# Performance work log

Hardware: AMD Instinct MI355X
Metric: run time of the kernel (lower is better)

## Reference

```python
import jax, jax.numpy as jnp
import numpy as np

B, S, D, GH = 8, 1024, 768, 32
THETA = 0.01


def _mlp(params, h):
    # DeepMemoryMLP (2 layers): Linear -> SiLU -> Linear
    W1, b1, W2, b2 = params
    h1 = jax.nn.silu(h @ W1.T + b1)
    return h1 @ W2.T + b2


def setup_inputs() -> dict:
    key = jax.random.key(0)
    ks = jax.random.split(key, 12)
    n = lambda k, sh, std=0.02: std * jax.random.normal(k, sh, dtype=jnp.float32)
    return {
        "x": jax.random.normal(ks[0], (B, S, D), dtype=jnp.float32),
        "WK_w": n(ks[1], (D, D)), "WK_b": jnp.zeros((D,), jnp.float32),
        "WV_w": n(ks[2], (D, D)), "WV_b": jnp.zeros((D,), jnp.float32),
        "WQ_w": n(ks[3], (D, D)), "WQ_b": jnp.zeros((D,), jnp.float32),
        "M_W1": n(ks[4], (D, D)), "M_b1": jnp.zeros((D,), jnp.float32),
        "M_W2": n(ks[5], (D, D)), "M_b2": jnp.zeros((D,), jnp.float32),
        "FG_W1": n(ks[6], (GH, D), std=float(1.0 / np.sqrt(D))), "FG_b1": jnp.zeros((GH,), jnp.float32),
        "FG_w2": n(ks[7], (1, GH), std=float(1.0 / np.sqrt(GH))), "FG_b2": jnp.zeros((1,), jnp.float32),
        "DG_W1": n(ks[8], (GH, D), std=float(1.0 / np.sqrt(D))), "DG_b1": jnp.zeros((GH,), jnp.float32),
        "DG_w2": n(ks[9], (1, GH), std=float(1.0 / np.sqrt(GH))), "DG_b2": jnp.zeros((1,), jnp.float32),
    }


def reference(x, WK_w, WK_b, WV_w, WV_b, WQ_w, WQ_b,
              M_W1, M_b1, M_W2, M_b2,
              FG_W1, FG_b1, FG_w2, FG_b2,
              DG_W1, DG_b1, DG_w2, DG_b2):
    # Projections (Eq. 12 inputs): k_t, v_t per token; q for retrieval
    k = jnp.einsum('bsd,ed->bse', x, WK_w) + WK_b   # [B,S,D]
    v = jnp.einsum('bsd,ed->bse', x, WV_w) + WV_b
    q = jnp.einsum('bsd,ed->bse', x, WQ_w) + WQ_b

    def gate(W1, b1, w2, b2):
        h = jax.nn.silu(jnp.einsum('bsd,hd->bsh', x, W1) + b1)
        return jax.nn.sigmoid(jnp.einsum('bsh,oh->bso', h, w2) + b2)[..., 0]  # [B,S]

    alpha = gate(FG_W1, FG_b1, FG_w2, FG_b2).mean(axis=0)  # [S] forget gate per step
    eta = gate(DG_W1, DG_b1, DG_w2, DG_b2).mean(axis=0)    # [S] momentum decay per step

    params0 = (M_W1, M_b1, M_W2, M_b2)
    S0 = jax.tree_util.tree_map(jnp.zeros_like, params0)   # momentum buffer

    def loss_fn(p, kt, vt):
        # l(M; x) = ||M(k_t) - v_t||^2 (MSE over the batch of tokens at step t)
        return jnp.mean((_mlp(p, kt) - vt) ** 2)

    def step(carry, inputs):
        p, s = carry
        kt, vt, a_t, e_t = inputs  # kt, vt: [B,D]
        g = jax.grad(loss_fn)(p, kt, vt)
        # Eq. 13: S_t = eta_t * S_{t-1} - theta * grad
        s = jax.tree_util.tree_map(lambda si, gi: e_t * si - THETA * gi, s, g)
        # Eq. 14: M_t = (1 - alpha_t) * M_{t-1} + S_t
        p = jax.tree_util.tree_map(lambda pi, si: (1.0 - a_t) * pi + si, p, s)
        return (p, s), None

    kt = jnp.swapaxes(k, 0, 1)  # [S,B,D]
    vt = jnp.swapaxes(v, 0, 1)
    (p_final, _), _ = jax.lax.scan(step, (params0, S0), (kt, vt, alpha, eta))

    # Retrieval with updated memory: out = M_T(q)
    return _mlp(p_final, q)
```

## Files before the change

kernel.cpp:

```cpp
#include <hip/hip_runtime.h>
#include <math.h>


#define S_LEN 1024
#define D_DIM 768
#define B_SZ 8
#define NWG 256
#define NTHR 192
#define THETA_F 0.01f
#define FLAG_STRIDE 16

__device__ __forceinline__ void st_agent(float* p, float v) {
  __hip_atomic_store(p, v, __ATOMIC_RELAXED, __HIP_MEMORY_SCOPE_AGENT);
}

template <int ACT, int REMAP>
__global__ __launch_bounds__(256) void gemm_tn(const float* __restrict__ A,
                                               const float* __restrict__ W,
                                               const float* __restrict__ bias,
                                               float* __restrict__ C) {
  __shared__ float As[16][132];
  __shared__ float Ws[16][68];
  const int tid = threadIdx.x;
  const int txx = tid & 15, tyy = tid >> 4;
  const int eb = blockIdx.x * 64;
  const int nb = blockIdx.y * 128;
  float acc[8][4];
#pragma unroll
  for (int i = 0; i < 8; ++i)
#pragma unroll
    for (int j = 0; j < 4; ++j) acc[i][j] = 0.f;

  const int lr = tid >> 2;
  const int lc = (tid & 3) << 2;

  for (int k0 = 0; k0 < 768; k0 += 16) {
    float4 a0 = *(const float4*)(A + (size_t)(nb + lr) * 768 + k0 + lc);
    float4 a1 = *(const float4*)(A + (size_t)(nb + lr + 64) * 768 + k0 + lc);
    float4 wv = *(const float4*)(W + (size_t)(eb + lr) * 768 + k0 + lc);
    __syncthreads();
    As[lc + 0][lr] = a0.x; As[lc + 1][lr] = a0.y; As[lc + 2][lr] = a0.z; As[lc + 3][lr] = a0.w;
    As[lc + 0][lr + 64] = a1.x; As[lc + 1][lr + 64] = a1.y; As[lc + 2][lr + 64] = a1.z; As[lc + 3][lr + 64] = a1.w;
    Ws[lc + 0][lr] = wv.x; Ws[lc + 1][lr] = wv.y; Ws[lc + 2][lr] = wv.z; Ws[lc + 3][lr] = wv.w;
    __syncthreads();
#pragma unroll
    for (int kk = 0; kk < 16; ++kk) {
      float4 x0 = *(const float4*)(&As[kk][tyy * 8]);
      float4 x1 = *(const float4*)(&As[kk][tyy * 8 + 4]);
      float4 y0 = *(const float4*)(&Ws[kk][txx * 4]);
      float a8[8] = {x0.x, x0.y, x0.z, x0.w, x1.x, x1.y, x1.z, x1.w};
      float b4[4] = {y0.x, y0.y, y0.z, y0.w};
#pragma unroll
      for (int i = 0; i < 8; ++i)
#pragma unroll
        for (int j = 0; j < 4; ++j) acc[i][j] = fmaf(a8[i], b4[j], acc[i][j]);
    }
  }
  float4 bv = *(const float4*)(bias + eb + txx * 4);
#pragma unroll
  for (int i = 0; i < 8; ++i) {
    int n = nb + tyy * 8 + i;
    float4 o;
    o.x = acc[i][0] + bv.x; o.y = acc[i][1] + bv.y;
    o.z = acc[i][2] + bv.z; o.w = acc[i][3] + bv.w;
    if (ACT == 1) {
      o.x = o.x / (1.f + expf(-o.x));
      o.y = o.y / (1.f + expf(-o.y));
      o.z = o.z / (1.f + expf(-o.z));
      o.w = o.w / (1.f + expf(-o.w));
    }
    size_t row = REMAP ? (size_t)((n & 1023) * 8 + (n >> 10)) : (size_t)n;
    *(float4*)(C + row * 768 + eb + txx * 4) = o;
  }
}

__global__ __launch_bounds__(512) void gates_kernel(
    const float* __restrict__ x, const float* __restrict__ FGW1,
    const float* __restrict__ FGb1, const float* __restrict__ FGw2,
    const float* __restrict__ FGb2, const float* __restrict__ DGW1,
    const float* __restrict__ DGb1, const float* __restrict__ DGw2,
    const float* __restrict__ DGb2, float* __restrict__ alphaA,
    float* __restrict__ etaA) {
  __shared__ float sA[8], sE[8];
  const int t = blockIdx.x, tid = threadIdx.x;
  const int b = tid >> 6, lane = tid & 63;
  const bool isFG = lane < 32;
  const int h = lane & 31;
  const float* xr = x + ((size_t)b * S_LEN + t) * D_DIM;
  const float* Wr = (isFG ? FGW1 : DGW1) + (size_t)h * D_DIM;
  float acc = 0.f;
  for (int d = 0; d < D_DIM; d += 4) {
    float4 xv = *(const float4*)(xr + d);
    float4 wv = *(const float4*)(Wr + d);
    acc = fmaf(xv.x, wv.x, acc);
    acc = fmaf(xv.y, wv.y, acc);
    acc = fmaf(xv.z, wv.z, acc);
    acc = fmaf(xv.w, wv.w, acc);
  }
  float z = acc + (isFG ? FGb1[h] : DGb1[h]);
  float sg = 1.f / (1.f + expf(-z));
  float p = z * sg * (isFG ? FGw2[h] : DGw2[h]);
#pragma unroll
  for (int off = 16; off > 0; off >>= 1) p += __shfl_xor(p, off, 64);
  if (lane == 0) sA[b] = 1.f / (1.f + expf(-(p + FGb2[0])));
  if (lane == 32) sE[b] = 1.f / (1.f + expf(-(p + DGb2[0])));
  __syncthreads();
  if (tid == 0) {
    float sa = 0.f, se = 0.f;
#pragma unroll
    for (int i = 0; i < 8; ++i) { sa += sA[i]; se += sE[i]; }
    alphaA[t] = sa * 0.125f;
    etaA[t] = se * 0.125f;
  }
}

__device__ __forceinline__ void grid_barrier(int* arrive, int* go, int wg,
                                             int tid, int epoch) {
  __syncthreads();
  if (wg == 0) {
#pragma unroll 1
    for (int s = tid + 1; s < NWG; s += NTHR) {
      while (__hip_atomic_load(arrive + s * FLAG_STRIDE, __ATOMIC_RELAXED,
                               __HIP_MEMORY_SCOPE_AGENT) < epoch) {
        __builtin_amdgcn_s_sleep(1);
      }
    }
    __syncthreads();
    if (tid == 0)
      __hip_atomic_store(go, epoch, __ATOMIC_RELAXED,
                         __HIP_MEMORY_SCOPE_AGENT);
  } else {
    if (tid == 0) {
      __hip_atomic_store(arrive + wg * FLAG_STRIDE, epoch, __ATOMIC_RELAXED,
                         __HIP_MEMORY_SCOPE_AGENT);
      while (__hip_atomic_load(go, __ATOMIC_RELAXED,
                               __HIP_MEMORY_SCOPE_AGENT) < epoch) {
        __builtin_amdgcn_s_sleep(1);
      }
    }
    __syncthreads();
  }
}

__device__ __forceinline__ void stage_tile(const float* gsrc, float* sdst,
                                           int tid) {
  const unsigned long long* src = (const unsigned long long*)gsrc;
  unsigned long long u[16];
#pragma unroll
  for (int j = 0; j < 16; ++j)
    u[j] = __hip_atomic_load(src + tid + j * 192, __ATOMIC_RELAXED,
                             __HIP_MEMORY_SCOPE_AGENT);
  unsigned long long* dst = (unsigned long long*)sdst;
#pragma unroll
  for (int j = 0; j < 16; ++j) dst[tid + j * 192] = u[j];
}

__global__ __launch_bounds__(NTHR, 1) void scan_kernel(
    const float* __restrict__ kbuf, const float* __restrict__ vbuf,
    const float* __restrict__ alphaA, const float* __restrict__ etaA,
    const float* __restrict__ MW1, const float* __restrict__ Mb1,
    const float* __restrict__ MW2, const float* __restrict__ Mb2,
    float* __restrict__ W1f, float* __restrict__ b1f, float* __restrict__ W2f,
    float* __restrict__ b2f, float* h1g, float* dOg,
    int* arrive, int* go) {
  __shared__ float sW1[3][768], sS1[3][768], sW2[3][768], sS2[3][768];
  __shared__ float sW2T[3][768], sS2T[3][768];
  __shared__ float sTile[6144];
  __shared__ float sb1[3], ssb1[3], sb2[3], ssb2[3];

  const int tid = threadIdx.x, wg = blockIdx.x;
  const int r = tid >> 6, lane = tid & 63;
  const int jg = wg * 3 + r;
  const int colb = lane * 12;

  {
    const float4* s1 = (const float4*)(MW1 + (size_t)jg * 768 + colb);
    float4* d1 = (float4*)(&sW1[r][colb]);
    d1[0] = s1[0]; d1[1] = s1[1]; d1[2] = s1[2];
    const float4* s2 = (const float4*)(MW2 + (size_t)jg * 768 + colb);
    float4* d2 = (float4*)(&sW2[r][colb]);
    d2[0] = s2[0]; d2[1] = s2[1]; d2[2] = s2[2];
#pragma unroll
    for (int m = 0; m < 12; ++m)
      sW2T[r][colb + m] = MW2[(size_t)(colb + m) * 768 + jg];
    float4 z4 = {0.f, 0.f, 0.f, 0.f};
    ((float4*)&sS1[r][colb])[0] = z4; ((float4*)&sS1[r][colb])[1] = z4; ((float4*)&sS1[r][colb])[2] = z4;
    ((float4*)&sS2[r][colb])[0] = z4; ((float4*)&sS2[r][colb])[1] = z4; ((float4*)&sS2[r][colb])[2] = z4;
    ((float4*)&sS2T[r][colb])[0] = z4; ((float4*)&sS2T[r][colb])[1] = z4; ((float4*)&sS2T[r][colb])[2] = z4;
    if (lane == 0) {
      sb1[r] = Mb1[jg]; sb2[r] = Mb2[jg];
      ssb1[r] = 0.f; ssb2[r] = 0.f;
    }
  }
  __syncthreads();

  int epoch = 0;
  alignas(16) float ktv[8][12];
  float hprev[8], sgv[8], h1loc[8];
  const float c0 = 2.0f / 6144.0f;

  for (int t = 0; t < S_LEN; ++t) {
    const float a_t = alphaA[t], e_t = etaA[t];
    const float om_a = 1.0f - a_t;

#pragma unroll
    for (int b = 0; b < 8; ++b) {
      const float4* kp =
          (const float4*)(kbuf + ((size_t)t * 8 + b) * 768 + colb);
      float4 k0 = kp[0], k1 = kp[1], k2 = kp[2];
      ktv[b][0] = k0.x; ktv[b][1] = k0.y; ktv[b][2] = k0.z; ktv[b][3] = k0.w;
      ktv[b][4] = k1.x; ktv[b][5] = k1.y; ktv[b][6] = k1.z; ktv[b][7] = k1.w;
      ktv[b][8] = k2.x; ktv[b][9] = k2.y; ktv[b][10] = k2.z; ktv[b][11] = k2.w;
    }

    {
      alignas(16) float w1v[12];
      const float4* wp = (const float4*)(&sW1[r][colb]);
      *(float4*)&w1v[0] = wp[0]; *(float4*)&w1v[4] = wp[1]; *(float4*)&w1v[8] = wp[2];
      float acc[8] = {0, 0, 0, 0, 0, 0, 0, 0};
#pragma unroll
      for (int m = 0; m < 12; ++m)
#pragma unroll
        for (int b = 0; b < 8; ++b) acc[b] = fmaf(ktv[b][m], w1v[m], acc[b]);
#pragma unroll
      for (int off = 32; off > 0; off >>= 1)
#pragma unroll
        for (int b = 0; b < 8; ++b) acc[b] += __shfl_xor(acc[b], off, 64);
      const float b1v = sb1[r];
#pragma unroll
      for (int b = 0; b < 8; ++b) {
        float z = acc[b] + b1v;
        float sg = 1.0f / (1.0f + expf(-z));
        hprev[b] = z; sgv[b] = sg; h1loc[b] = z * sg;
      }
#pragma unroll
      for (int b = 0; b < 8; ++b)
        if (lane == b) st_agent(h1g + b * 768 + jg, h1loc[b]);
    }
    grid_barrier(arrive, go, wg, tid, ++epoch);

    {
      stage_tile(h1g, sTile, tid);
      __syncthreads();
      alignas(16) float w2v[12];
      const float4* wp = (const float4*)(&sW2[r][colb]);
      *(float4*)&w2v[0] = wp[0]; *(float4*)&w2v[4] = wp[1]; *(float4*)&w2v[8] = wp[2];
      alignas(16) float hc[8][12];
#pragma unroll
      for (int b = 0; b < 8; ++b) {
        const float4* hp = (const float4*)(&sTile[b * 768 + colb]);
        float4 h0 = hp[0], h1 = hp[1], h2 = hp[2];
        hc[b][0] = h0.x; hc[b][1] = h0.y; hc[b][2] = h0.z; hc[b][3] = h0.w;
        hc[b][4] = h1.x; hc[b][5] = h1.y; hc[b][6] = h1.z; hc[b][7] = h1.w;
        hc[b][8] = h2.x; hc[b][9] = h2.y; hc[b][10] = h2.z; hc[b][11] = h2.w;
      }
      float acc[8] = {0, 0, 0, 0, 0, 0, 0, 0};
#pragma unroll
      for (int m = 0; m < 12; ++m)
#pragma unroll
        for (int b = 0; b < 8; ++b) acc[b] = fmaf(hc[b][m], w2v[m], acc[b]);
#pragma unroll
      for (int off = 32; off > 0; off >>= 1)
#pragma unroll
        for (int b = 0; b < 8; ++b) acc[b] += __shfl_xor(acc[b], off, 64);
      const float b2v = sb2[r];
      float dOv[8];
#pragma unroll
      for (int b = 0; b < 8; ++b) {
        float outv = acc[b] + b2v;
        dOv[b] = c0 * (outv - vbuf[((size_t)t * 8 + b) * 768 + jg]);
      }
#pragma unroll
      for (int b = 0; b < 8; ++b)
        if (lane == b) st_agent(dOg + b * 768 + jg, dOv[b]);
#pragma unroll
      for (int m = 0; m < 12; ++m) {
        float g = 0.f;
#pragma unroll
        for (int b = 0; b < 8; ++b) g = fmaf(dOv[b], hc[b][m], g);
        float snew = e_t * sS2[r][colb + m] - THETA_F * g;
        sS2[r][colb + m] = snew;
        sW2[r][colb + m] = om_a * w2v[m] + snew;
      }
      if (lane == 0) {
        float gb = dOv[0] + dOv[1] + dOv[2] + dOv[3] + dOv[4] + dOv[5] + dOv[6] + dOv[7];
        float snew = e_t * ssb2[r] - THETA_F * gb;
        ssb2[r] = snew;
        sb2[r] = om_a * sb2[r] + snew;
      }
    }
    grid_barrier(arrive, go, wg, tid, ++epoch);

    {
      stage_tile(dOg, sTile, tid);
      __syncthreads();
      alignas(16) float w2tv[12];
      const float4* wp = (const float4*)(&sW2T[r][colb]);
      *(float4*)&w2tv[0] = wp[0]; *(float4*)&w2tv[4] = wp[1]; *(float4*)&w2tv[8] = wp[2];
      alignas(16) float dc[8][12];
#pragma unroll
      for (int b = 0; b < 8; ++b) {
        const float4* dp = (const float4*)(&sTile[b * 768 + colb]);
        float4 d0 = dp[0], d1 = dp[1], d2 = dp[2];
        dc[b][0] = d0.x; dc[b][1] = d0.y; dc[b][2] = d0.z; dc[b][3] = d0.w;
        dc[b][4] = d1.x; dc[b][5] = d1.y; dc[b][6] = d1.z; dc[b][7] = d1.w;
        dc[b][8] = d2.x; dc[b][9] = d2.y; dc[b][10] = d2.z; dc[b][11] = d2.w;
      }
      float acc[8] = {0, 0, 0, 0, 0, 0, 0, 0};
#pragma unroll
      for (int m = 0; m < 12; ++m)
#pragma unroll
        for (int b = 0; b < 8; ++b) acc[b] = fmaf(dc[b][m], w2tv[m], acc[b]);
#pragma unroll
      for (int off = 32; off > 0; off >>= 1)
#pragma unroll
        for (int b = 0; b < 8; ++b) acc[b] += __shfl_xor(acc[b], off, 64);
      float dpre[8];
#pragma unroll
      for (int b = 0; b < 8; ++b)
        dpre[b] = acc[b] * (sgv[b] * (1.0f + hprev[b] * (1.0f - sgv[b])));
#pragma unroll
      for (int m = 0; m < 12; ++m) {
        float g = 0.f;
#pragma unroll
        for (int b = 0; b < 8; ++b) g = fmaf(dpre[b], ktv[b][m], g);
        float snew = e_t * sS1[r][colb + m] - THETA_F * g;
        sS1[r][colb + m] = snew;
        sW1[r][colb + m] = om_a * sW1[r][colb + m] + snew;
      }
#pragma unroll
      for (int m = 0; m < 12; ++m) {
        float g = 0.f;
#pragma unroll
        for (int b = 0; b < 8; ++b) g = fmaf(h1loc[b], dc[b][m], g);
        float snew = e_t * sS2T[r][colb + m] - THETA_F * g;
        sS2T[r][colb + m] = snew;
        sW2T[r][colb + m] = om_a * sW2T[r][colb + m] + snew;
      }
      if (lane == 0) {
        float gb = dpre[0] + dpre[1] + dpre[2] + dpre[3] + dpre[4] + dpre[5] + dpre[6] + dpre[7];
        float snew = e_t * ssb1[r] - THETA_F * gb;
        ssb1[r] = snew;
        sb1[r] = om_a * sb1[r] + snew;
      }
    }
  }

  {
    float4* d1 = (float4*)(W1f + (size_t)jg * 768 + colb);
    const float4* s1 = (const float4*)(&sW1[r][colb]);
    d1[0] = s1[0]; d1[1] = s1[1]; d1[2] = s1[2];
    float4* d2 = (float4*)(W2f + (size_t)jg * 768 + colb);
    const float4* s2 = (const float4*)(&sW2[r][colb]);
    d2[0] = s2[0]; d2[1] = s2[1]; d2[2] = s2[2];
    if (lane == 0) {
      b1f[jg] = sb1[r];
      b2f[jg] = sb2[r];
    }
  }
}

extern "C" void kernel_launch(void* const* d_in, const int* in_sizes, int n_in,
                              void* d_out, int out_size, void* d_ws,
                              size_t ws_size, hipStream_t stream) {
  (void)in_sizes; (void)n_in; (void)out_size; (void)ws_size;
  const float* x   = (const float*)d_in[0];
  const float* WKw = (const float*)d_in[1];
  const float* WKb = (const float*)d_in[2];
  const float* WVw = (const float*)d_in[3];
  const float* WVb = (const float*)d_in[4];
  const float* WQw = (const float*)d_in[5];
  const float* WQb = (const float*)d_in[6];
  const float* MW1 = (const float*)d_in[7];
  const float* Mb1 = (const float*)d_in[8];
  const float* MW2 = (const float*)d_in[9];
  const float* Mb2 = (const float*)d_in[10];
  const float* FGW1 = (const float*)d_in[11];
  const float* FGb1 = (const float*)d_in[12];
  const float* FGw2 = (const float*)d_in[13];
  const float* FGb2 = (const float*)d_in[14];
  const float* DGW1 = (const float*)d_in[15];
  const float* DGb1 = (const float*)d_in[16];
  const float* DGw2 = (const float*)d_in[17];
  const float* DGb2 = (const float*)d_in[18];
  float* out = (float*)d_out;

  float* ws = (float*)d_ws;
  float* kbuf = ws;
  float* vbuf = ws + 6291456;
  float* W1f  = ws + 12582912;
  float* W2f  = W1f + 589824;
  float* b1f  = W2f + 589824;
  float* b2f  = b1f + 768;
  float* alphaA = b2f + 768;
  float* etaA   = alphaA + 1024;
  float* h1g  = etaA + 1024;
  float* dOg  = h1g + 6144;
  int* arrive = (int*)(dOg + 6144);
  int* go     = arrive + NWG * FLAG_STRIDE;
  float* qbuf = kbuf;
  float* h1q  = vbuf;

  hipMemsetAsync(arrive, 0, (NWG * FLAG_STRIDE + FLAG_STRIDE) * sizeof(int),
                 stream);

  dim3 gg(12, 64), bb(256);
  gemm_tn<0, 1><<<gg, bb, 0, stream>>>(x, WKw, WKb, kbuf);
  gemm_tn<0, 1><<<gg, bb, 0, stream>>>(x, WVw, WVb, vbuf);
  gates_kernel<<<dim3(1024), dim3(512), 0, stream>>>(
      x, FGW1, FGb1, FGw2, FGb2, DGW1, DGb1, DGw2, DGb2, alphaA, etaA);
  scan_kernel<<<dim3(NWG), dim3(NTHR), 0, stream>>>(
      kbuf, vbuf, alphaA, etaA, MW1, Mb1, MW2, Mb2, W1f, b1f, W2f, b2f, h1g,
      dOg, arrive, go);
  gemm_tn<0, 0><<<gg, bb, 0, stream>>>(x, WQw, WQb, qbuf);
  gemm_tn<1, 0><<<gg, bb, 0, stream>>>(qbuf, W1f, b1f, h1q);
  gemm_tn<0, 0><<<gg, bb, 0, stream>>>(h1q, W2f, b2f, out);
}
```

Before: 12.57 ms.

## Keep per-row memory weights and momentum in registers with fewer, larger workgroups

The persistent scan kernel now keeps each wavefront's slice of W1, W2, W2ᵀ and their momentum buffers in registers instead of shared memory. It launches 128 workgroups of 384 threads (6 rows each) instead of 256 of 192, which halves the number of participants in every grid barrier. k_t is re-read from global memory in the backward step rather than held in registers, to limit register pressure. This removes the shared-memory traffic for weight updates and cuts barrier fan-in, at the cost of higher register use per thread and an extra global read of k each step.

```diff
diff --git a/kernel.cpp b/kernel.cpp
--- a/kernel.cpp
+++ b/kernel.cpp
@@ -5,13 +5,26 @@
 #define S_LEN 1024
 #define D_DIM 768
 #define B_SZ 8
-#define NWG 256
-#define NTHR 192
+#define NWG 128
+#define NTHR 384
 #define THETA_F 0.01f
 #define FLAG_STRIDE 16
 
 __device__ __forceinline__ void st_agent(float* p, float v) {
   __hip_atomic_store(p, v, __ATOMIC_RELAXED, __HIP_MEMORY_SCOPE_AGENT);
+}
+
+__device__ __forceinline__ void load12(const float* __restrict__ p, float* d) {
+  float4 a = ((const float4*)p)[0], b = ((const float4*)p)[1],
+         c = ((const float4*)p)[2];
+  d[0]=a.x; d[1]=a.y; d[2]=a.z; d[3]=a.w;
+  d[4]=b.x; d[5]=b.y; d[6]=b.z; d[7]=b.w;
+  d[8]=c.x; d[9]=c.y; d[10]=c.z; d[11]=c.w;
+}
+__device__ __forceinline__ void store12(float* __restrict__ p, const float* s) {
+  ((float4*)p)[0] = make_float4(s[0], s[1], s[2], s[3]);
+  ((float4*)p)[1] = make_float4(s[4], s[5], s[6], s[7]);
+  ((float4*)p)[2] = make_float4(s[8], s[9], s[10], s[11]);
 }
 
 template <int ACT, int REMAP>
@@ -145,14 +158,14 @@
 __device__ __forceinline__ void stage_tile(const float* gsrc, float* sdst,
                                            int tid) {
   const unsigned long long* src = (const unsigned long long*)gsrc;
-  unsigned long long u[16];
-#pragma unroll
-  for (int j = 0; j < 16; ++j)
-    u[j] = __hip_atomic_load(src + tid + j * 192, __ATOMIC_RELAXED,
+  unsigned long long u[8];
+#pragma unroll
+  for (int j = 0; j < 8; ++j)
+    u[j] = __hip_atomic_load(src + tid + j * NTHR, __ATOMIC_RELAXED,
                              __HIP_MEMORY_SCOPE_AGENT);
   unsigned long long* dst = (unsigned long long*)sdst;
 #pragma unroll
-  for (int j = 0; j < 16; ++j) dst[tid + j * 192] = u[j];
+  for (int j = 0; j < 8; ++j) dst[tid + j * NTHR] = u[j];
 }
 
 __global__ __launch_bounds__(NTHR, 1) void scan_kernel(
@@ -163,39 +176,24 @@
     float* __restrict__ W1f, float* __restrict__ b1f, float* __restrict__ W2f,
     float* __restrict__ b2f, float* h1g, float* dOg,
     int* arrive, int* go) {
-  __shared__ float sW1[3][768], sS1[3][768], sW2[3][768], sS2[3][768];
-  __shared__ float sW2T[3][768], sS2T[3][768];
   __shared__ float sTile[6144];
-  __shared__ float sb1[3], ssb1[3], sb2[3], ssb2[3];
 
   const int tid = threadIdx.x, wg = blockIdx.x;
-  const int r = tid >> 6, lane = tid & 63;
-  const int jg = wg * 3 + r;
+  const int w = tid >> 6, lane = tid & 63;
+  const int jg = wg * 6 + w;
   const int colb = lane * 12;
 
-  {
-    const float4* s1 = (const float4*)(MW1 + (size_t)jg * 768 + colb);
-    float4* d1 = (float4*)(&sW1[r][colb]);
-    d1[0] = s1[0]; d1[1] = s1[1]; d1[2] = s1[2];
-    const float4* s2 = (const float4*)(MW2 + (size_t)jg * 768 + colb);
-    float4* d2 = (float4*)(&sW2[r][colb]);
-    d2[0] = s2[0]; d2[1] = s2[1]; d2[2] = s2[2];
-#pragma unroll
-    for (int m = 0; m < 12; ++m)
-      sW2T[r][colb + m] = MW2[(size_t)(colb + m) * 768 + jg];
-    float4 z4 = {0.f, 0.f, 0.f, 0.f};
-    ((float4*)&sS1[r][colb])[0] = z4; ((float4*)&sS1[r][colb])[1] = z4; ((float4*)&sS1[r][colb])[2] = z4;
-    ((float4*)&sS2[r][colb])[0] = z4; ((float4*)&sS2[r][colb])[1] = z4; ((float4*)&sS2[r][colb])[2] = z4;
-    ((float4*)&sS2T[r][colb])[0] = z4; ((float4*)&sS2T[r][colb])[1] = z4; ((float4*)&sS2T[r][colb])[2] = z4;
-    if (lane == 0) {
-      sb1[r] = Mb1[jg]; sb2[r] = Mb2[jg];
-      ssb1[r] = 0.f; ssb2[r] = 0.f;
-    }
-  }
-  __syncthreads();
+  float w1[12], s1[12], w2[12], s2[12], w2t[12], s2t[12];
+  load12(MW1 + (size_t)jg * 768 + colb, w1);
+  load12(MW2 + (size_t)jg * 768 + colb, w2);
+#pragma unroll
+  for (int m = 0; m < 12; ++m) {
+    w2t[m] = MW2[(size_t)(colb + m) * 768 + jg];
+    s1[m] = 0.f; s2[m] = 0.f; s2t[m] = 0.f;
+  }
+  float b1v = Mb1[jg], b2v = Mb2[jg], sb1v = 0.f, sb2v = 0.f;
 
   int epoch = 0;
-  alignas(16) float ktv[8][12];
   float hprev[8], sgv[8], h1loc[8];
   const float c0 = 2.0f / 6144.0f;
 
@@ -203,30 +201,21 @@
     const float a_t = alphaA[t], e_t = etaA[t];
     const float om_a = 1.0f - a_t;
 
-#pragma unroll
-    for (int b = 0; b < 8; ++b) {
-      const float4* kp =
-          (const float4*)(kbuf + ((size_t)t * 8 + b) * 768 + colb);
-      float4 k0 = kp[0], k1 = kp[1], k2 = kp[2];
-      ktv[b][0] = k0.x; ktv[b][1] = k0.y; ktv[b][2] = k0.z; ktv[b][3] = k0.w;
-      ktv[b][4] = k1.x; ktv[b][5] = k1.y; ktv[b][6] = k1.z; ktv[b][7] = k1.w;
-      ktv[b][8] = k2.x; ktv[b][9] = k2.y; ktv[b][10] = k2.z; ktv[b][11] = k2.w;
-    }
-
     {
-      alignas(16) float w1v[12];
-      const float4* wp = (const float4*)(&sW1[r][colb]);
-      *(float4*)&w1v[0] = wp[0]; *(float4*)&w1v[4] = wp[1]; *(float4*)&w1v[8] = wp[2];
-      float acc[8] = {0, 0, 0, 0, 0, 0, 0, 0};
-#pragma unroll
-      for (int m = 0; m < 12; ++m)
-#pragma unroll
-        for (int b = 0; b < 8; ++b) acc[b] = fmaf(ktv[b][m], w1v[m], acc[b]);
+      float acc[8];
+#pragma unroll
+      for (int b = 0; b < 8; ++b) {
+        float kv[12];
+        load12(kbuf + ((size_t)t * 8 + b) * 768 + colb, kv);
+        float a = 0.f;
+#pragma unroll
+        for (int m = 0; m < 12; ++m) a = fmaf(kv[m], w1[m], a);
+        acc[b] = a;
+      }
 #pragma unroll
       for (int off = 32; off > 0; off >>= 1)
 #pragma unroll
         for (int b = 0; b < 8; ++b) acc[b] += __shfl_xor(acc[b], off, 64);
-      const float b1v = sb1[r];
 #pragma unroll
       for (int b = 0; b < 8; ++b) {
         float z = acc[b] + b1v;
@@ -242,75 +231,62 @@
     {
       stage_tile(h1g, sTile, tid);
       __syncthreads();
-      alignas(16) float w2v[12];
-      const float4* wp = (const float4*)(&sW2[r][colb]);
-      *(float4*)&w2v[0] = wp[0]; *(float4*)&w2v[4] = wp[1]; *(float4*)&w2v[8] = wp[2];
-      alignas(16) float hc[8][12];
-#pragma unroll
-      for (int b = 0; b < 8; ++b) {
-        const float4* hp = (const float4*)(&sTile[b * 768 + colb]);
-        float4 h0 = hp[0], h1 = hp[1], h2 = hp[2];
-        hc[b][0] = h0.x; hc[b][1] = h0.y; hc[b][2] = h0.z; hc[b][3] = h0.w;
-        hc[b][4] = h1.x; hc[b][5] = h1.y; hc[b][6] = h1.z; hc[b][7] = h1.w;
-        hc[b][8] = h2.x; hc[b][9] = h2.y; hc[b][10] = h2.z; hc[b][11] = h2.w;
-      }
-      float acc[8] = {0, 0, 0, 0, 0, 0, 0, 0};
-#pragma unroll
-      for (int m = 0; m < 12; ++m)
-#pragma unroll
-        for (int b = 0; b < 8; ++b) acc[b] = fmaf(hc[b][m], w2v[m], acc[b]);
+      float acc[8];
+#pragma unroll
+      for (int b = 0; b < 8; ++b) {
+        float hv[12];
+        load12(&sTile[b * 768 + colb], hv);
+        float a = 0.f;
+#pragma unroll
+        for (int m = 0; m < 12; ++m) a = fmaf(hv[m], w2[m], a);
+        acc[b] = a;
+      }
 #pragma unroll
       for (int off = 32; off > 0; off >>= 1)
 #pragma unroll
         for (int b = 0; b < 8; ++b) acc[b] += __shfl_xor(acc[b], off, 64);
-      const float b2v = sb2[r];
       float dOv[8];
 #pragma unroll
       for (int b = 0; b < 8; ++b) {
         float outv = acc[b] + b2v;
         dOv[b] = c0 * (outv - vbuf[((size_t)t * 8 + b) * 768 + jg]);
-      }
-#pragma unroll
-      for (int b = 0; b < 8; ++b)
         if (lane == b) st_agent(dOg + b * 768 + jg, dOv[b]);
+      }
+      float gm[12];
+#pragma unroll
+      for (int m = 0; m < 12; ++m) gm[m] = 0.f;
+#pragma unroll
+      for (int b = 0; b < 8; ++b) {
+        float hv[12];
+        load12(&sTile[b * 768 + colb], hv);
+#pragma unroll
+        for (int m = 0; m < 12; ++m) gm[m] = fmaf(dOv[b], hv[m], gm[m]);
+      }
 #pragma unroll
       for (int m = 0; m < 12; ++m) {
-        float g = 0.f;
-#pragma unroll
-        for (int b = 0; b < 8; ++b) g = fmaf(dOv[b], hc[b][m], g);
-        float snew = e_t * sS2[r][colb + m] - THETA_F * g;
-        sS2[r][colb + m] = snew;
-        sW2[r][colb + m] = om_a * w2v[m] + snew;
-      }
-      if (lane == 0) {
-        float gb = dOv[0] + dOv[1] + dOv[2] + dOv[3] + dOv[4] + dOv[5] + dOv[6] + dOv[7];
-        float snew = e_t * ssb2[r] - THETA_F * gb;
-        ssb2[r] = snew;
-        sb2[r] = om_a * sb2[r] + snew;
-      }
+        s2[m] = e_t * s2[m] - THETA_F * gm[m];
+        w2[m] = om_a * w2[m] + s2[m];
+      }
+      float gb = dOv[0] + dOv[1] + dOv[2] + dOv[3] + dOv[4] + dOv[5] +
+                 dOv[6] + dOv[7];
+      sb2v = e_t * sb2v - THETA_F * gb;
+      b2v = om_a * b2v + sb2v;
     }
     grid_barrier(arrive, go, wg, tid, ++epoch);
 
     {
       stage_tile(dOg, sTile, tid);
       __syncthreads();
-      alignas(16) float w2tv[12];
-      const float4* wp = (const float4*)(&sW2T[r][colb]);
-      *(float4*)&w2tv[0] = wp[0]; *(float4*)&w2tv[4] = wp[1]; *(float4*)&w2tv[8] = wp[2];
-      alignas(16) float dc[8][12];
-#pragma unroll
-      for (int b = 0; b < 8; ++b) {
-        const float4* dp = (const float4*)(&sTile[b * 768 + colb]);
-        float4 d0 = dp[0], d1 = dp[1], d2 = dp[2];
-        dc[b][0] = d0.x; dc[b][1] = d0.y; dc[b][2] = d0.z; dc[b][3] = d0.w;
-        dc[b][4] = d1.x; dc[b][5] = d1.y; dc[b][6] = d1.z; dc[b][7] = d1.w;
-        dc[b][8] = d2.x; dc[b][9] = d2.y; dc[b][10] = d2.z; dc[b][11] = d2.w;
-      }
-      float acc[8] = {0, 0, 0, 0, 0, 0, 0, 0};
-#pragma unroll
-      for (int m = 0; m < 12; ++m)
-#pragma unroll
-        for (int b = 0; b < 8; ++b) acc[b] = fmaf(dc[b][m], w2tv[m], acc[b]);
+      float acc[8];
+#pragma unroll
+      for (int b = 0; b < 8; ++b) {
+        float dv[12];
+        load12(&sTile[b * 768 + colb], dv);
+        float a = 0.f;
+#pragma unroll
+        for (int m = 0; m < 12; ++m) a = fmaf(dv[m], w2t[m], a);
+        acc[b] = a;
+      }
 #pragma unroll
       for (int off = 32; off > 0; off >>= 1)
 #pragma unroll
@@ -319,44 +295,47 @@
 #pragma unroll
       for (int b = 0; b < 8; ++b)
         dpre[b] = acc[b] * (sgv[b] * (1.0f + hprev[b] * (1.0f - sgv[b])));
+      float gm[12];
+#pragma unroll
+      for (int m = 0; m < 12; ++m) gm[m] = 0.f;
+#pragma unroll
+      for (int b = 0; b < 8; ++b) {
+        float kv[12];
+        load12(kbuf + ((size_t)t * 8 + b) * 768 + colb, kv);
+#pragma unroll
+        for (int m = 0; m < 12; ++m) gm[m] = fmaf(dpre[b], kv[m], gm[m]);
+      }
 #pragma unroll
       for (int m = 0; m < 12; ++m) {
-        float g = 0.f;
-#pragma unroll
-        for (int b = 0; b < 8; ++b) g = fmaf(dpre[b], ktv[b][m], g);
-        float snew = e_t * sS1[r][colb + m] - THETA_F * g;
-        sS1[r][colb + m] = snew;
-        sW1[r][colb + m] = om_a * sW1[r][colb + m] + snew;
+        s1[m] = e_t * s1[m] - THETA_F * gm[m];
+        w1[m] = om_a * w1[m] + s1[m];
+      }
+#pragma unroll
+      for (int m = 0; m < 12; ++m) gm[m] = 0.f;
+#pragma unroll
+      for (int b = 0; b < 8; ++b) {
+        float dv[12];
+        load12(&sTile[b * 768 + colb], dv);
+#pragma unroll
+        for (int m = 0; m < 12; ++m) gm[m] = fmaf(h1loc[b], dv[m], gm[m]);
       }
 #pragma unroll
       for (int m = 0; m < 12; ++m) {
-        float g = 0.f;
-#pragma unroll
-        for (int b = 0; b < 8; ++b) g = fmaf(h1loc[b], dc[b][m], g);
-        float snew = e_t * sS2T[r][colb + m] - THETA_F * g;
-        sS2T[r][colb + m] = snew;
-        sW2T[r][colb + m] = om_a * sW2T[r][colb + m] + snew;
-      }
-      if (lane == 0) {
-        float gb = dpre[0] + dpre[1] + dpre[2] + dpre[3] + dpre[4] + dpre[5] + dpre[6] + dpre[7];
-        float snew = e_t * ssb1[r] - THETA_F * gb;
-        ssb1[r] = snew;
-        sb1[r] = om_a * sb1[r] + snew;
-      }
-    }
-  }
-
-  {
-    float4* d1 = (float4*)(W1f + (size_t)jg * 768 + colb);
-    const float4* s1 = (const float4*)(&sW1[r][colb]);
-    d1[0] = s1[0]; d1[1] = s1[1]; d1[2] = s1[2];
-    float4* d2 = (float4*)(W2f + (size_t)jg * 768 + colb);
-    const float4* s2 = (const float4*)(&sW2[r][colb]);
-    d2[0] = s2[0]; d2[1] = s2[1]; d2[2] = s2[2];
-    if (lane == 0) {
-      b1f[jg] = sb1[r];
-      b2f[jg] = sb2[r];
-    }
+        s2t[m] = e_t * s2t[m] - THETA_F * gm[m];
+        w2t[m] = om_a * w2t[m] + s2t[m];
+      }
+      float gb = dpre[0] + dpre[1] + dpre[2] + dpre[3] + dpre[4] + dpre[5] +
+                 dpre[6] + dpre[7];
+      sb1v = e_t * sb1v - THETA_F * gb;
+      b1v = om_a * b1v + sb1v;
+    }
+  }
+
+  store12(W1f + (size_t)jg * 768 + colb, w1);
+  store12(W2f + (size_t)jg * 768 + colb, w2);
+  if (lane == 0) {
+    b1f[jg] = b1v;
+    b2f[jg] = b2v;
   }
 }
 
```

Measured after the change: 24.08 ms. 1.92x slower.
